# Performance work log

Measured on AMD Instinct MI355X. Metric: run time of the kernel, lower is better.

Reference implementation:

```python
import jax, jax.numpy as jnp
import numpy as np

HEADS = 8
DIM_HEAD = 64
SCALE = DIM_HEAD ** -0.5


def setup_inputs() -> dict:
    key = jax.random.key(0)
    ks = jax.random.split(key, 8)
    B, Nq, Dq = 4, 2048, 512
    Nk, Dc = 1024, 768
    inner = HEADS * DIM_HEAD  # 512
    x = jax.random.normal(ks[0], (B, Nq, Dq), dtype=jnp.float32)
    context = jax.random.normal(ks[1], (B, Nk, Dc), dtype=jnp.float32)
    # Linear weights stored [in, out]; y = x @ W (+ b)
    Wq = jax.random.normal(ks[2], (Dq, inner), dtype=jnp.float32) / np.sqrt(Dq)
    Wk = jax.random.normal(ks[3], (Dc, inner), dtype=jnp.float32) / np.sqrt(Dc)
    Wv = jax.random.normal(ks[4], (Dc, inner), dtype=jnp.float32) / np.sqrt(Dc)
    Wo = jax.random.normal(ks[5], (inner, Dq), dtype=jnp.float32) / np.sqrt(inner)
    bo = jax.random.normal(ks[6], (Dq,), dtype=jnp.float32) * 0.01
    return {"x": x, "context": context, "Wq": Wq, "Wk": Wk, "Wv": Wv, "Wo": Wo, "bo": bo}


def reference(x, context, Wq, Wk, Wv, Wo, bo):
    B, Nq, _ = x.shape
    Nk = context.shape[1]
    # projections
    q = x @ Wq          # [B, Nq, h*d]
    k = context @ Wk    # [B, Nk, h*d]
    v = context @ Wv    # [B, Nk, h*d]
    # split heads: b n (h d) -> b h n d
    q = q.reshape(B, Nq, HEADS, DIM_HEAD).transpose(0, 2, 1, 3)
    k = k.reshape(B, Nk, HEADS, DIM_HEAD).transpose(0, 2, 1, 3)
    v = v.reshape(B, Nk, HEADS, DIM_HEAD).transpose(0, 2, 1, 3)
    # fp32 QK^T (ATTN_PRECISION == 'fp32' path)
    sim = jnp.einsum('bhid,bhjd->bhij', q.astype(jnp.float32), k.astype(jnp.float32)) * SCALE
    attn = jax.nn.softmax(sim, axis=-1)
    out = jnp.einsum('bhij,bhjd->bhid', attn, v)  # [B, h, Nq, d]
    out = out.transpose(0, 2, 1, 3).reshape(B, Nq, HEADS * DIM_HEAD)
    return out @ Wo + bo  # dropout=0 -> identity
```

## Files before the change

kernel.cpp:

```cpp
#include <hip/hip_runtime.h>
#include <cstddef>
#include <cstdint>

typedef __attribute__((ext_vector_type(8))) short bf16x8;
typedef __attribute__((ext_vector_type(4))) float f32x4;

static __device__ __forceinline__ short f2bf(float f) {
    union { float f; unsigned u; } x;
    x.f = f;
    unsigned r = (x.u + 0x7FFFu + ((x.u >> 16) & 1u)) >> 16;
    return (short)r;
}

typedef __attribute__((address_space(3))) unsigned lds_u;
typedef const __attribute__((address_space(1))) unsigned glb_u;
static __device__ __forceinline__ void gld_lds16(const void* g, void* l) {
    __builtin_amdgcn_global_load_lds((glb_u*)g, (lds_u*)l, 16, 0, 0);
}

__global__ __launch_bounds__(256) void convert_kernel(
    const float* __restrict__ x, const float* __restrict__ c,
    short* __restrict__ xb, short* __restrict__ cb, int n1, int n2)
{
    int i = blockIdx.x * 256 + threadIdx.x;
    int nn1 = n1 >> 2;
    const float* src; short* dst; int off;
    if (i < nn1) { src = x; dst = xb; off = i; }
    else { src = c; dst = cb; off = i - nn1; if (off >= (n2 >> 2)) return; }
    float4 v = ((const float4*)src)[off];
    ushort4 w;
    w.x = (unsigned short)f2bf(v.x); w.y = (unsigned short)f2bf(v.y);
    w.z = (unsigned short)f2bf(v.z); w.w = (unsigned short)f2bf(v.w);
    ((ushort4*)dst)[off] = w;
}

__global__ __launch_bounds__(256) void wtrans_kernel(
    const float* __restrict__ Wq, const float* __restrict__ Wk,
    const float* __restrict__ Wv, const float* __restrict__ Wo,
    short* __restrict__ wqT, short* __restrict__ wkvT, short* __restrict__ woT)
{
    __shared__ float T[32][33];
    const int z = blockIdx.z;
    const float* src; short* dst; int R;
    if (z == 0)      { src = Wq; dst = wqT;  R = 512; }
    else if (z == 1) { src = Wk; dst = wkvT; R = 768; }
    else if (z == 2) { src = Wv; dst = wkvT + (size_t)512 * 768; R = 768; }
    else             { src = Wo; dst = woT;  R = 512; }
    const int yt = blockIdx.y;
    if (yt * 32 >= R) return;
    const int xt = blockIdx.x;
    const int tid = threadIdx.x;
    {
        int r = tid >> 3, c4 = (tid & 7) * 4;
        float4 v = *(const float4*)&src[(size_t)(yt * 32 + r) * 512 + xt * 32 + c4];
        T[r][c4] = v.x; T[r][c4 + 1] = v.y; T[r][c4 + 2] = v.z; T[r][c4 + 3] = v.w;
    }
    __syncthreads();
    {
        int cc = tid >> 3, r4 = (tid & 7) * 4;
        ushort4 w;
        w.x = (unsigned short)f2bf(T[r4][cc]);     w.y = (unsigned short)f2bf(T[r4 + 1][cc]);
        w.z = (unsigned short)f2bf(T[r4 + 2][cc]); w.w = (unsigned short)f2bf(T[r4 + 3][cc]);
        *(ushort4*)&dst[(size_t)(xt * 32 + cc) * R + yt * 32 + r4] = w;
    }
}

__global__ __launch_bounds__(256) void vtrans_kernel(
    const short* __restrict__ v, short* __restrict__ vT)
{
    __shared__ short T[32][33];
    const int b = blockIdx.z, yt = blockIdx.y, xt = blockIdx.x;
    const int tid = threadIdx.x;
    {
        int r = tid >> 3, c4 = (tid & 7) * 4;
        ushort4 vv = *(const ushort4*)&v[((size_t)(b * 1024 + yt * 32 + r)) * 1024 + xt * 32 + c4];
        T[r][c4] = (short)vv.x; T[r][c4 + 1] = (short)vv.y;
        T[r][c4 + 2] = (short)vv.z; T[r][c4 + 3] = (short)vv.w;
    }
    __syncthreads();
    {
        int cc = tid >> 3, r4 = (tid & 7) * 4;
        ushort4 w;
        w.x = (unsigned short)T[r4][cc];     w.y = (unsigned short)T[r4 + 1][cc];
        w.z = (unsigned short)T[r4 + 2][cc]; w.w = (unsigned short)T[r4 + 3][cc];
        *(ushort4*)&vT[((size_t)(b * 512 + xt * 32 + cc)) * 1024 + yt * 32 + r4] = w;
    }
}

static __device__ __forceinline__ void gemm_core(
    const short* __restrict__ A, const short* __restrict__ BT, int K,
    int bm, int bn, short* As, short* Bs, f32x4 acc[4][4])
{
    const int tid  = threadIdx.x;
    const int lane = tid & 63;
    const int wave = tid >> 6;
    const int lm   = lane & 15;
    const int quad = lane >> 4;
    const int wm = (wave >> 1) * 64;
    const int wn = (wave & 1) * 64;
    const int c = tid >> 7, r = tid & 127;

    {
        const short* Ag = &A[(size_t)(bm + r) * K];
        const short* Bg = &BT[(size_t)(bn + r) * K];
        gld_lds16(Ag + c * 8,       &As[tid * 8]);
        gld_lds16(Ag + (c + 2) * 8, &As[(tid + 256) * 8]);
        gld_lds16(Bg + c * 8,       &Bs[tid * 8]);
        gld_lds16(Bg + (c + 2) * 8, &Bs[(tid + 256) * 8]);
    }

    for (int k0 = 0, it = 0; k0 < K; k0 += 32, ++it) {
        short* Ac = As + (it & 1) * 4096;
        short* Bc = Bs + (it & 1) * 4096;
        __syncthreads();
        if (k0 + 32 < K) {
            short* An = As + ((it & 1) ^ 1) * 4096;
            short* Bn = Bs + ((it & 1) ^ 1) * 4096;
            const short* Ag = &A[(size_t)(bm + r) * K + k0 + 32];
            const short* Bg = &BT[(size_t)(bn + r) * K + k0 + 32];
            gld_lds16(Ag + c * 8,       &An[tid * 8]);
            gld_lds16(Ag + (c + 2) * 8, &An[(tid + 256) * 8]);
            gld_lds16(Bg + c * 8,       &Bn[tid * 8]);
            gld_lds16(Bg + (c + 2) * 8, &Bn[(tid + 256) * 8]);
        }
        bf16x8 af[4], bfr[4];
        #pragma unroll
        for (int i = 0; i < 4; ++i)
            af[i] = *(const bf16x8*)&Ac[(quad * 128 + wm + i * 16 + lm) * 8];
        #pragma unroll
        for (int j = 0; j < 4; ++j)
            bfr[j] = *(const bf16x8*)&Bc[(quad * 128 + wn + j * 16 + lm) * 8];
        #pragma unroll
        for (int i = 0; i < 4; ++i)
            #pragma unroll
            for (int j = 0; j < 4; ++j)
                acc[i][j] = __builtin_amdgcn_mfma_f32_16x16x32_bf16(
                    af[i], bfr[j], acc[i][j], 0, 0, 0);
    }
}

__global__ __launch_bounds__(256) void qkv_kernel(
    const short* __restrict__ xb, const short* __restrict__ cb,
    const short* __restrict__ wqT, const short* __restrict__ wkvT,
    short* __restrict__ qb, short* __restrict__ kvb)
{
    __shared__ short As[2 * 4096];
    __shared__ short Bs[2 * 4096];
    const int bid = blockIdx.x;
    const short *A, *BT; short* C; int K, ldc, bm, bn;
    if (bid < 256) { A = xb; BT = wqT;  C = qb;  K = 512; ldc = 512;
                     bm = (bid >> 2) * 128; bn = (bid & 3) * 128; }
    else { int b2 = bid - 256; A = cb; BT = wkvT; C = kvb; K = 768; ldc = 1024;
           bm = (b2 >> 3) * 128; bn = (b2 & 7) * 128; }

    f32x4 acc[4][4] = {};
    gemm_core(A, BT, K, bm, bn, As, Bs, acc);

    const int lane = threadIdx.x & 63, wave = threadIdx.x >> 6;
    const int lm = lane & 15, quad = lane >> 4;
    const int wm = (wave >> 1) * 64, wn = (wave & 1) * 64;
    #pragma unroll
    for (int j = 0; j < 4; ++j) {
        int col = bn + wn + j * 16 + lm;
        #pragma unroll
        for (int i = 0; i < 4; ++i) {
            int row0 = bm + wm + i * 16 + quad * 4;
            #pragma unroll
            for (int r = 0; r < 4; ++r)
                C[(size_t)(row0 + r) * ldc + col] = f2bf(acc[i][j][r]);
        }
    }
}

__global__ __launch_bounds__(256) void ogemm_kernel(
    const short* __restrict__ ob, const short* __restrict__ woT,
    const float* __restrict__ bias, float* __restrict__ out)
{
    __shared__ short As[2 * 4096];
    __shared__ short Bs[2 * 4096];
    const int bid = blockIdx.x;
    const int bm = (bid >> 2) * 128, bn = (bid & 3) * 128;

    f32x4 acc[4][4] = {};
    gemm_core(ob, woT, 512, bm, bn, As, Bs, acc);

    const int lane = threadIdx.x & 63, wave = threadIdx.x >> 6;
    const int lm = lane & 15, quad = lane >> 4;
    const int wm = (wave >> 1) * 64, wn = (wave & 1) * 64;
    #pragma unroll
    for (int j = 0; j < 4; ++j) {
        int col = bn + wn + j * 16 + lm;
        float bv = bias[col];
        #pragma unroll
        for (int i = 0; i < 4; ++i) {
            int row0 = bm + wm + i * 16 + quad * 4;
            #pragma unroll
            for (int r = 0; r < 4; ++r)
                out[(size_t)(row0 + r) * 512 + col] = acc[i][j][r] + bv;
        }
    }
}

__global__ __launch_bounds__(256) void attn_kernel(
    const short* __restrict__ q, const short* __restrict__ k,
    const short* __restrict__ vT, short* __restrict__ o)
{
    __shared__ short Qs[4096];
    __shared__ short Ks[2 * 4096];
    __shared__ short Vs[2 * 4096];

    const int tid  = threadIdx.x;
    const int lane = tid & 63;
    const int wave = tid >> 6;
    const int lm   = lane & 15;
    const int quad = lane >> 4;
    const int qt = blockIdx.x, h = blockIdx.y, b = blockIdx.z;
    const size_t qrow0 = (size_t)b * 2048 + qt * 64;
    const size_t krow0 = (size_t)b * 1024;
    const int hcol = h * 64;
    const size_t vrow0 = ((size_t)b * 8 + h) * 64;
    const int sc = tid >> 6, sr = tid & 63;

    #pragma unroll
    for (int p = 0; p < 2; ++p) {
        int idx = p * 256 + tid;
        int c = idx >> 6, r = idx & 63;
        gld_lds16(&q[(qrow0 + r) * 512 + hcol + c * 8], &Qs[idx * 8]);
        gld_lds16(&k[(krow0 + r) * 1024 + hcol + c * 8], &Ks[idx * 8]);
        gld_lds16(&vT[(vrow0 + r) * 1024 + c * 8], &Vs[idx * 8]);
    }
    __syncthreads();
    bf16x8 qf0 = *(const bf16x8*)&Qs[((0 + quad) * 64 + wave * 16 + lm) * 8];
    bf16x8 qf1 = *(const bf16x8*)&Qs[((4 + quad) * 64 + wave * 16 + lm) * 8];

    short* Pw = &Qs[wave * 1024];
    const int pr0 = lm * 64 + ((quad ^ (lm & 7)) << 3);
    const int pr1 = lm * 64 + (((quad + 4) ^ (lm & 7)) << 3);

    constexpr float C1 = 0.18033688f;
    constexpr float C2 = 11.5415603f;

    f32x4 oacc[4] = {};
    float lrow[4] = {0.0f, 0.0f, 0.0f, 0.0f};

    for (int t = 0; t < 16; ++t) {
        const short* Kc = &Ks[(t & 1) * 4096];
        const short* Vc = &Vs[(t & 1) * 4096];
        __syncthreads();
        if (t + 1 < 16) {
            short* Kn = &Ks[((t & 1) ^ 1) * 4096];
            short* Vn = &Vs[((t & 1) ^ 1) * 4096];
            #pragma unroll
            for (int p = 0; p < 2; ++p) {
                int idx = p * 256 + tid;
                int c = idx >> 6, r = idx & 63;
                gld_lds16(&k[(krow0 + (t + 1) * 64 + r) * 1024 + hcol + c * 8], &Kn[idx * 8]);
                gld_lds16(&vT[(vrow0 + r) * 1024 + (t + 1) * 64 + c * 8], &Vn[idx * 8]);
            }
        }

        f32x4 sacc[4] = {};
        #pragma unroll
        for (int j = 0; j < 4; ++j) {
            bf16x8 kf0 = *(const bf16x8*)&Kc[((0 + quad) * 64 + j * 16 + lm) * 8];
            bf16x8 kf1 = *(const bf16x8*)&Kc[((4 + quad) * 64 + j * 16 + lm) * 8];
            sacc[j] = __builtin_amdgcn_mfma_f32_16x16x32_bf16(qf0, kf0, sacc[j], 0, 0, 0);
            sacc[j] = __builtin_amdgcn_mfma_f32_16x16x32_bf16(qf1, kf1, sacc[j], 0, 0, 0);
        }

        #pragma unroll
        for (int r = 0; r < 4; ++r) {
            int row = quad * 4 + r;
            int rsw = (row & 7);
            float lsum = 0.0f;
            #pragma unroll
            for (int j = 0; j < 4; ++j) {
                float pv = exp2f(fmaf(sacc[j][r], C1, -C2));
                lsum += pv;
                int cc = (2 * j + (lm >> 3)) ^ rsw;
                Pw[row * 64 + (cc << 3) + (lm & 7)] = f2bf(pv);
            }
            lrow[r] += lsum;
        }
        bf16x8 pf0 = *(const bf16x8*)&Pw[pr0];
        bf16x8 pf1 = *(const bf16x8*)&Pw[pr1];

        #pragma unroll
        for (int j = 0; j < 4; ++j) {
            bf16x8 vf0 = *(const bf16x8*)&Vc[((0 + quad) * 64 + j * 16 + lm) * 8];
            bf16x8 vf1 = *(const bf16x8*)&Vc[((4 + quad) * 64 + j * 16 + lm) * 8];
            oacc[j] = __builtin_amdgcn_mfma_f32_16x16x32_bf16(pf0, vf0, oacc[j], 0, 0, 0);
            oacc[j] = __builtin_amdgcn_mfma_f32_16x16x32_bf16(pf1, vf1, oacc[j], 0, 0, 0);
        }
    }

    float inv[4];
    #pragma unroll
    for (int r = 0; r < 4; ++r) {
        float s = lrow[r];
        #pragma unroll
        for (int d = 1; d < 16; d <<= 1) s += __shfl_xor(s, d);
        inv[r] = 1.0f / s;
    }
    #pragma unroll
    for (int j = 0; j < 4; ++j) {
        int col = hcol + j * 16 + lm;
        #pragma unroll
        for (int r = 0; r < 4; ++r) {
            size_t row = qrow0 + wave * 16 + quad * 4 + r;
            o[row * 512 + col] = f2bf(oacc[j][r] * inv[r]);
        }
    }
}

extern "C" void kernel_launch(void* const* d_in, const int* in_sizes, int n_in,
                              void* d_out, int out_size, void* d_ws, size_t ws_size,
                              hipStream_t stream)
{
    const float* x   = (const float*)d_in[0];
    const float* ctx = (const float*)d_in[1];
    const float* Wq  = (const float*)d_in[2];
    const float* Wk  = (const float*)d_in[3];
    const float* Wv  = (const float*)d_in[4];
    const float* Wo  = (const float*)d_in[5];
    const float* bo  = (const float*)d_in[6];

    char* ws = (char*)d_ws;
    short* xb   = (short*)(ws);
    short* cb   = (short*)(ws + (8u << 20));
    short* wqT  = (short*)(ws + (14u << 20));
    short* wkvT = (short*)(ws + (14u << 20) + (512u << 10));
    short* woT  = (short*)(ws + (16u << 20));
    short* qb   = (short*)(ws + (16u << 20) + (512u << 10));
    short* kvb  = (short*)(ws + (24u << 20) + (512u << 10));
    short* ob   = xb;
    short* vT   = cb;

    convert_kernel<<<7168, 256, 0, stream>>>(x, ctx, xb, cb, 8192 * 512, 4096 * 768);
    wtrans_kernel<<<dim3(16, 24, 4), 256, 0, stream>>>(Wq, Wk, Wv, Wo, wqT, wkvT, woT);
    qkv_kernel<<<512, 256, 0, stream>>>(xb, cb, wqT, wkvT, qb, kvb);
    vtrans_kernel<<<dim3(16, 32, 4), 256, 0, stream>>>(kvb + 512, vT);
    attn_kernel<<<dim3(32, 8, 4), 256, 0, stream>>>(qb, kvb, vT, ob);
    ogemm_kernel<<<256, 256, 0, stream>>>(ob, woT, bo, (float*)d_out);
}
```

Before: 184.0 us.

## Compute transposed scores so P stays in registers, permuting V layout to match

The attention kernel now computes S^T = K·Q^T, so each lane's MFMA output already matches the A-operand layout of the P·V MFMA. That removes the LDS round-trip for P and the Q staging buffer. To make this work, the V-transpose kernel writes keys in a permuted order matching the register packing of P, and the exp/convert path uses the hardware exp2 and a packed bf16 conversion. It also loads Q fragments straight from global memory, adds s_setprio around the MFMA blocks, and simplifies the row-sum reduction. The risk is a layout mismatch between the permuted V and the packed P, which would give wrong results.

```diff
diff --git a/kernel.cpp b/kernel.cpp
--- a/kernel.cpp
+++ b/kernel.cpp
@@ -83,7 +83,11 @@
         ushort4 w;
         w.x = (unsigned short)T[r4][cc];     w.y = (unsigned short)T[r4 + 1][cc];
         w.z = (unsigned short)T[r4 + 2][cc]; w.w = (unsigned short)T[r4 + 3][cc];
-        *(ushort4*)&vT[((size_t)(b * 512 + xt * 32 + cc)) * 1024 + yt * 32 + r4] = w;
+        int kk = yt * 32 + r4;
+        int kl = kk & 63;
+        int g  = ((kl >> 5) << 2) | ((kl >> 2) & 3);
+        int p  = (kk & ~63) | (g << 3) | (((kl >> 4) & 1) << 2);
+        *(ushort4*)&vT[((size_t)(b * 512 + xt * 32 + cc)) * 1024 + p] = w;
     }
 }
 
@@ -205,7 +209,6 @@
     const short* __restrict__ q, const short* __restrict__ k,
     const short* __restrict__ vT, short* __restrict__ o)
 {
-    __shared__ short Qs[4096];
     __shared__ short Ks[2 * 4096];
     __shared__ short Vs[2 * 4096];
 
@@ -219,96 +222,95 @@
     const size_t krow0 = (size_t)b * 1024;
     const int hcol = h * 64;
     const size_t vrow0 = ((size_t)b * 8 + h) * 64;
-    const int sc = tid >> 6, sr = tid & 63;
-
-    #pragma unroll
-    for (int p = 0; p < 2; ++p) {
-        int idx = p * 256 + tid;
-        int c = idx >> 6, r = idx & 63;
-        gld_lds16(&q[(qrow0 + r) * 512 + hcol + c * 8], &Qs[idx * 8]);
-        gld_lds16(&k[(krow0 + r) * 1024 + hcol + c * 8], &Ks[idx * 8]);
-        gld_lds16(&vT[(vrow0 + r) * 1024 + c * 8], &Vs[idx * 8]);
-    }
-    __syncthreads();
-    bf16x8 qf0 = *(const bf16x8*)&Qs[((0 + quad) * 64 + wave * 16 + lm) * 8];
-    bf16x8 qf1 = *(const bf16x8*)&Qs[((4 + quad) * 64 + wave * 16 + lm) * 8];
-
-    short* Pw = &Qs[wave * 1024];
-    const int pr0 = lm * 64 + ((quad ^ (lm & 7)) << 3);
-    const int pr1 = lm * 64 + (((quad + 4) ^ (lm & 7)) << 3);
+
+    const short* kg = &k[(krow0 + (tid & 63)) * 1024 + hcol + (tid >> 6) * 8];
+    const short* vg = &vT[(vrow0 + (tid & 63)) * 1024 + (tid >> 6) * 8];
+
+    gld_lds16(kg,      &Ks[tid * 8]);
+    gld_lds16(kg + 32, &Ks[(tid + 256) * 8]);
+    gld_lds16(vg,      &Vs[tid * 8]);
+    gld_lds16(vg + 32, &Vs[(tid + 256) * 8]);
+    kg += 64 * 1024; vg += 64;
+
+    const short* qrow = &q[(qrow0 + wave * 16 + lm) * 512 + hcol];
+    const bf16x8 qf0 = *(const bf16x8*)&qrow[quad * 8];
+    const bf16x8 qf1 = *(const bf16x8*)&qrow[32 + quad * 8];
 
     constexpr float C1 = 0.18033688f;
     constexpr float C2 = 11.5415603f;
 
     f32x4 oacc[4] = {};
-    float lrow[4] = {0.0f, 0.0f, 0.0f, 0.0f};
+    float lsum = 0.0f;
+
+    const int fro = (quad * 64 + lm) * 8;
 
     for (int t = 0; t < 16; ++t) {
-        const short* Kc = &Ks[(t & 1) * 4096];
-        const short* Vc = &Vs[(t & 1) * 4096];
+        const short* Kc = &Ks[(t & 1) * 4096 + fro];
+        const short* Vc = &Vs[(t & 1) * 4096 + fro];
         __syncthreads();
-        if (t + 1 < 16) {
+        if (t < 15) {
             short* Kn = &Ks[((t & 1) ^ 1) * 4096];
             short* Vn = &Vs[((t & 1) ^ 1) * 4096];
+            gld_lds16(kg,      &Kn[tid * 8]);
+            gld_lds16(kg + 32, &Kn[(tid + 256) * 8]);
+            gld_lds16(vg,      &Vn[tid * 8]);
+            gld_lds16(vg + 32, &Vn[(tid + 256) * 8]);
+            kg += 64 * 1024; vg += 64;
+        }
+
+        f32x4 sacc[4] = {};
+        __builtin_amdgcn_s_setprio(1);
+        #pragma unroll
+        for (int j = 0; j < 4; ++j) {
+            bf16x8 kf0 = *(const bf16x8*)&Kc[(j * 16) * 8];
+            bf16x8 kf1 = *(const bf16x8*)&Kc[(256 + j * 16) * 8];
+            sacc[j] = __builtin_amdgcn_mfma_f32_16x16x32_bf16(kf0, qf0, sacc[j], 0, 0, 0);
+            sacc[j] = __builtin_amdgcn_mfma_f32_16x16x32_bf16(kf1, qf1, sacc[j], 0, 0, 0);
+        }
+        __builtin_amdgcn_s_setprio(0);
+
+        union { unsigned u[4]; bf16x8 v; } pf0, pf1;
+        #pragma unroll
+        for (int j = 0; j < 4; ++j) {
             #pragma unroll
-            for (int p = 0; p < 2; ++p) {
-                int idx = p * 256 + tid;
-                int c = idx >> 6, r = idx & 63;
-                gld_lds16(&k[(krow0 + (t + 1) * 64 + r) * 1024 + hcol + c * 8], &Kn[idx * 8]);
-                gld_lds16(&vT[(vrow0 + r) * 1024 + (t + 1) * 64 + c * 8], &Vn[idx * 8]);
+            for (int rp = 0; rp < 2; ++rp) {
+                float p0 = __builtin_amdgcn_exp2f(fmaf(sacc[j][2 * rp],     C1, -C2));
+                float p1 = __builtin_amdgcn_exp2f(fmaf(sacc[j][2 * rp + 1], C1, -C2));
+                lsum += p0 + p1;
+                unsigned pr;
+                asm("v_cvt_pk_bf16_f32 %0, %1, %2" : "=v"(pr) : "v"(p0), "v"(p1));
+                if (j < 2) pf0.u[j * 2 + rp] = pr;
+                else       pf1.u[(j - 2) * 2 + rp] = pr;
             }
         }
 
-        f32x4 sacc[4] = {};
+        __builtin_amdgcn_s_setprio(1);
         #pragma unroll
         for (int j = 0; j < 4; ++j) {
-            bf16x8 kf0 = *(const bf16x8*)&Kc[((0 + quad) * 64 + j * 16 + lm) * 8];
-            bf16x8 kf1 = *(const bf16x8*)&Kc[((4 + quad) * 64 + j * 16 + lm) * 8];
-            sacc[j] = __builtin_amdgcn_mfma_f32_16x16x32_bf16(qf0, kf0, sacc[j], 0, 0, 0);
-            sacc[j] = __builtin_amdgcn_mfma_f32_16x16x32_bf16(qf1, kf1, sacc[j], 0, 0, 0);
-        }
-
-        #pragma unroll
-        for (int r = 0; r < 4; ++r) {
-            int row = quad * 4 + r;
-            int rsw = (row & 7);
-            float lsum = 0.0f;
-            #pragma unroll
-            for (int j = 0; j < 4; ++j) {
-                float pv = exp2f(fmaf(sacc[j][r], C1, -C2));
-                lsum += pv;
-                int cc = (2 * j + (lm >> 3)) ^ rsw;
-                Pw[row * 64 + (cc << 3) + (lm & 7)] = f2bf(pv);
-            }
-            lrow[r] += lsum;
-        }
-        bf16x8 pf0 = *(const bf16x8*)&Pw[pr0];
-        bf16x8 pf1 = *(const bf16x8*)&Pw[pr1];
-
-        #pragma unroll
-        for (int j = 0; j < 4; ++j) {
-            bf16x8 vf0 = *(const bf16x8*)&Vc[((0 + quad) * 64 + j * 16 + lm) * 8];
-            bf16x8 vf1 = *(const bf16x8*)&Vc[((4 + quad) * 64 + j * 16 + lm) * 8];
-            oacc[j] = __builtin_amdgcn_mfma_f32_16x16x32_bf16(pf0, vf0, oacc[j], 0, 0, 0);
-            oacc[j] = __builtin_amdgcn_mfma_f32_16x16x32_bf16(pf1, vf1, oacc[j], 0, 0, 0);
-        }
-    }
-
-    float inv[4];
+            bf16x8 vf0 = *(const bf16x8*)&Vc[(j * 16) * 8];
+            bf16x8 vf1 = *(const bf16x8*)&Vc[(256 + j * 16) * 8];
+            oacc[j] = __builtin_amdgcn_mfma_f32_16x16x32_bf16(pf0.v, vf0, oacc[j], 0, 0, 0);
+            oacc[j] = __builtin_amdgcn_mfma_f32_16x16x32_bf16(pf1.v, vf1, oacc[j], 0, 0, 0);
+        }
+        __builtin_amdgcn_s_setprio(0);
+    }
+
+    float s = lsum;
+    s += __shfl_xor(s, 16);
+    s += __shfl_xor(s, 32);
+    const float inv = 1.0f / s;
+    float invr[4];
     #pragma unroll
-    for (int r = 0; r < 4; ++r) {
-        float s = lrow[r];
-        #pragma unroll
-        for (int d = 1; d < 16; d <<= 1) s += __shfl_xor(s, d);
-        inv[r] = 1.0f / s;
-    }
+    for (int r = 0; r < 4; ++r)
+        invr[r] = __shfl(inv, quad * 20 + r);
+
     #pragma unroll
     for (int j = 0; j < 4; ++j) {
         int col = hcol + j * 16 + lm;
         #pragma unroll
         for (int r = 0; r < 4; ++r) {
             size_t row = qrow0 + wave * 16 + quad * 4 + r;
-            o[row * 512 + col] = f2bf(oacc[j][r] * inv[r]);
+            o[row * 512 + col] = f2bf(oacc[j][r] * invr[r]);
         }
     }
 }
```

Result: no change. 182.8 us (-0.6%).
